# Kernel optimization log

Hardware: AMD Instinct MI355X
Metric: run time of the kernel (lower is better)

The kernel has to match this reference:

```python
import jax, jax.numpy as jnp
import numpy as np

B, D_IN, D_H, D_OUT = 1024, 1024, 4096, 1024
SPARSITY = 0.5  # fraction of weights KEPT (top-k)


def setup_inputs() -> dict:
    key = jax.random.key(0)
    ks = jax.random.split(key, 13)
    def kaiming(k, shape):
        fan_in = shape[-1] if len(shape) > 1 else shape[0]
        bound = 1.0 / np.sqrt(fan_in)
        return jax.random.uniform(k, shape, jnp.float32, -bound, bound)
    inp = {
        "x":   jax.random.normal(ks[0], (B, D_IN), jnp.float32),
        "W1":  kaiming(ks[1], (D_H, D_IN)),
        "b1":  kaiming(ks[2], (D_H,)),
        "W2":  kaiming(ks[3], (D_H, D_H)),
        "b2":  kaiming(ks[4], (D_H,)),
        "W3":  kaiming(ks[5], (D_OUT, D_H)),
        "b3":  kaiming(ks[6], (D_OUT,)),
        # scores: kaiming-uniform for weights, N(0, 0.01) for biases (as in Mask.__init__)
        "sW1": kaiming(ks[7], (D_H, D_IN)),
        "sb1": 0.01 * jax.random.normal(ks[8], (D_H,), jnp.float32),
        "sW2": kaiming(ks[9], (D_H, D_H)),
        "sb2": 0.01 * jax.random.normal(ks[10], (D_H,), jnp.float32),
        "sW3": kaiming(ks[11], (D_OUT, D_H)),
        "sb3": 0.01 * jax.random.normal(ks[12], (D_OUT,), jnp.float32),
    }
    return inp


def _global_masks(scores):
    """Single fused global top-k threshold mask (replaces O(P) redundant sorts).
    Bottom (1-SPARSITY) fraction (by value rank) -> 0, top SPARSITY fraction -> 1."""
    flat = jnp.concatenate([s.ravel() for s in scores])
    n = flat.shape[0]
    j = int((1.0 - SPARSITY) * n)  # number of zeroed entries
    idx = jnp.argsort(flat)
    bin_mask = jnp.zeros((n,), flat.dtype).at[idx[j:]].set(1.0)
    # straight-through: d(mask)/d(score) = 1 (GetSubnet_global.backward returns g)
    st_mask = bin_mask + flat - jax.lax.stop_gradient(flat)
    sizes = [int(np.prod(s.shape)) for s in scores]
    offs = np.concatenate([[0], np.cumsum(sizes)])
    return [st_mask[offs[i]:offs[i + 1]].reshape(scores[i].shape)
            for i in range(len(scores))]


def reference(x, W1, b1, W2, b2, W3, b3, sW1, sb1, sW2, sb2, sW3, sb3):
    masks = _global_masks([sW1, sb1, sW2, sb2, sW3, sb3])
    mW1, mb1, mW2, mb2, mW3, mb3 = masks
    # masked params, then MLP forward (torch Linear: y = x @ W.T + b)
    h = jax.nn.relu(x @ (W1 * mW1).T + b1 * mb1)
    h = jax.nn.relu(h @ (W2 * mW2).T + b2 * mb2)
    return h @ (W3 * mW3).T + b3 * mb3
```

## Files before the change

kernel.cpp:

```cpp
#include <hip/hip_runtime.h>
#include <hip/hip_bf16.h>
#include <stdint.h>


typedef __bf16 bf16_t;
typedef __bf16 bf16x4 __attribute__((ext_vector_type(4)));
typedef __bf16 bf16x8 __attribute__((ext_vector_type(8)));
typedef float  f32x4  __attribute__((ext_vector_type(4)));

using gvoid = const __attribute__((address_space(1))) void;
using svoid = __attribute__((address_space(3))) void;

#define O1 4194304L
#define O2 4198400L
#define O3 20975616L
#define O4 20979712L
#define O5 25174016L
#define N_TOT 25175040L
#define J_RANK 12587520u
#define CAND_CAP 4096

#define WS_HIST 0u
#define WS_RES  32768u
#define WS_CNT  32784u
#define WS_CAND 32800u
#define WS_W1B  131072u
#define WS_B1F  8519680u
#define WS_W2B  8536064u
#define WS_B2F  42090496u
#define WS_W3B  42106880u
#define WS_B3F  50495488u
#define WS_H1F  50511872u
#define WS_H2F  58900480u
#define WS_FAST_END 67289088ull
#define WS_H1   131072u
#define WS_H2   8519680u

#define SWZ(row, chunk) ((((chunk) + ((row) >> 1)) & 3))

__device__ __forceinline__ unsigned int mono32(float f) {
    unsigned int u = __float_as_uint(f);
    return (u & 0x80000000u) ? ~u : (u | 0x80000000u);
}

__global__ __launch_bounds__(256) void zero_kernel(unsigned int* p, int n) {
    int i = blockIdx.x * 256 + threadIdx.x;
    if (i < n) p[i] = 0u;
}

__device__ __forceinline__ void seg_lookup(long e,
    const float* s0, const float* s1, const float* s2,
    const float* s3, const float* s4, const float* s5,
    const float** sp, long* off) {
    if (e < O1)      { *sp = s0; *off = e; }
    else if (e < O2) { *sp = s1; *off = e - O1; }
    else if (e < O3) { *sp = s2; *off = e - O2; }
    else if (e < O4) { *sp = s3; *off = e - O3; }
    else if (e < O5) { *sp = s4; *off = e - O4; }
    else             { *sp = s5; *off = e - O5; }
}

__global__ __launch_bounds__(256) void hist_kernel(
    const float* s0, const float* s1, const float* s2,
    const float* s3, const float* s4, const float* s5,
    unsigned int* hist) {
    __shared__ unsigned int lh[8192];
    for (int i = threadIdx.x; i < 8192; i += 256) lh[i] = 0u;
    __syncthreads();
    const long ng = N_TOT / 4;
    for (long g = (long)blockIdx.x * 256 + threadIdx.x; g < ng;
         g += (long)gridDim.x * 256) {
        long e = g * 4;
        const float* sp; long o;
        seg_lookup(e, s0, s1, s2, s3, s4, s5, &sp, &o);
        float4 v = *(const float4*)(sp + o);
        atomicAdd(&lh[mono32(v.x) >> 19], 1u);
        atomicAdd(&lh[mono32(v.y) >> 19], 1u);
        atomicAdd(&lh[mono32(v.z) >> 19], 1u);
        atomicAdd(&lh[mono32(v.w) >> 19], 1u);
    }
    __syncthreads();
    for (int i = threadIdx.x; i < 8192; i += 256) {
        unsigned int c = lh[i];
        if (c) atomicAdd(&hist[i], c);
    }
}

__global__ __launch_bounds__(256) void select_kernel(const unsigned int* hist,
                                                     unsigned int* res) {
    __shared__ unsigned int part[256];
    int tid = threadIdx.x;
    unsigned int s = 0;
    for (int b = tid * 32; b < tid * 32 + 32; ++b) s += hist[b];
    part[tid] = s;
    __syncthreads();
    if (tid == 0) {
        unsigned int acc = 0;
        for (int i = 0; i < 256; ++i) { unsigned int v = part[i]; part[i] = acc; acc += v; }
    }
    __syncthreads();
    unsigned int acc = part[tid];
    for (int b = tid * 32; b < tid * 32 + 32; ++b) {
        unsigned int h = hist[b];
        if (acc <= J_RANK && J_RANK < acc + h) {
            res[0] = (unsigned int)b;
            res[1] = acc;
            res[2] = J_RANK - acc;
        }
        acc += h;
    }
}

__global__ __launch_bounds__(256) void mask_apply_fast(
    const float* s0, const float* s1, const float* s2,
    const float* s3, const float* s4, const float* s5,
    const float* w0, const float* w1, const float* w2,
    const float* w3, const float* w4, const float* w5,
    bf16_t* W1b, float* b1f, bf16_t* W2b, float* b2f, bf16_t* W3b, float* b3f,
    const unsigned int* res, unsigned int* cand_cnt, unsigned long long* cand) {
    const unsigned int C = res[0];
    const long ng = N_TOT / 4;
    for (long g = (long)blockIdx.x * 256 + threadIdx.x; g < ng;
         g += (long)gridDim.x * 256) {
        long e = g * 4;
        const float* sp; long o;
        seg_lookup(e, s0, s1, s2, s3, s4, s5, &sp, &o);
        const float* wp;
        if (e < O1)      wp = w0;
        else if (e < O2) wp = w1;
        else if (e < O3) wp = w2;
        else if (e < O4) wp = w3;
        else if (e < O5) wp = w4;
        else             wp = w5;
        float4 sv = *(const float4*)(sp + o);
        float4 wv = *(const float4*)(wp + o);
#define PROC(comp, ci)                                                         \
        { unsigned int key = mono32(sv.comp); unsigned int kb = key >> 19;     \
          if (kb < C) wv.comp = 0.f;                                           \
          else if (kb == C) {                                                  \
              unsigned int slot = atomicAdd(cand_cnt, 1u);                     \
              if (slot < CAND_CAP)                                             \
                  cand[slot] = (((unsigned long long)key) << 32) |             \
                               (unsigned long long)(unsigned int)(e + ci);     \
          } }
        PROC(x, 0) PROC(y, 1) PROC(z, 2) PROC(w, 3)
#undef PROC
        if (e < O1) {
            bf16x4 b; b[0]=(__bf16)wv.x; b[1]=(__bf16)wv.y; b[2]=(__bf16)wv.z; b[3]=(__bf16)wv.w;
            *(bf16x4*)(W1b + o) = b;
        } else if (e < O2) {
            *(float4*)(b1f + o) = wv;
        } else if (e < O3) {
            bf16x4 b; b[0]=(__bf16)wv.x; b[1]=(__bf16)wv.y; b[2]=(__bf16)wv.z; b[3]=(__bf16)wv.w;
            *(bf16x4*)(W2b + o) = b;
        } else if (e < O4) {
            *(float4*)(b2f + o) = wv;
        } else if (e < O5) {
            bf16x4 b; b[0]=(__bf16)wv.x; b[1]=(__bf16)wv.y; b[2]=(__bf16)wv.z; b[3]=(__bf16)wv.w;
            *(bf16x4*)(W3b + o) = b;
        } else {
            *(float4*)(b3f + o) = wv;
        }
    }
}

__global__ __launch_bounds__(256) void finalize_fast(
    const unsigned int* res, const unsigned int* cand_cnt,
    const unsigned long long* cand,
    bf16_t* W1b, float* b1f, bf16_t* W2b, float* b2f, bf16_t* W3b, float* b3f) {
    __shared__ unsigned long long buf[CAND_CAP];
    int tid = threadIdx.x;
    unsigned int cnt = *cand_cnt; if (cnt > CAND_CAP) cnt = CAND_CAP;
    unsigned int need = res[2];   if (need > cnt) need = cnt;
    for (int i = tid; i < (int)cnt; i += 256) buf[i] = cand[i];
    __syncthreads();
    for (int i = tid; i < (int)cnt; i += 256) {
        unsigned long long me = buf[i];
        unsigned int rank = 0;
        for (unsigned int j = 0; j < cnt; ++j) rank += (buf[j] < me);
        if (rank < need) {
            long idx = (long)(unsigned int)(me & 0xFFFFFFFFu);
            if (idx < O1)      W1b[idx] = (__bf16)0.f;
            else if (idx < O2) b1f[idx - O1] = 0.f;
            else if (idx < O3) W2b[idx - O2] = (__bf16)0.f;
            else if (idx < O4) b2f[idx - O3] = 0.f;
            else if (idx < O5) W3b[idx - O4] = (__bf16)0.f;
            else               b3f[idx - O5] = 0.f;
        }
    }
}

__global__ __launch_bounds__(256) void mask_apply_kernel(
    const float* s0, const float* s1, const float* s2,
    const float* s3, const float* s4, const float* s5,
    float* w0, float* w1, float* w2, float* w3, float* w4, float* w5,
    const unsigned int* res, unsigned int* cand_cnt, unsigned long long* cand) {
    const unsigned int C = res[0];
    const long ng = N_TOT / 4;
    for (long g = (long)blockIdx.x * 256 + threadIdx.x; g < ng;
         g += (long)gridDim.x * 256) {
        long e = g * 4;
        const float* sp; long o;
        seg_lookup(e, s0, s1, s2, s3, s4, s5, &sp, &o);
        float* wp;
        if (e < O1)      wp = w0;
        else if (e < O2) wp = w1;
        else if (e < O3) wp = w2;
        else if (e < O4) wp = w3;
        else if (e < O5) wp = w4;
        else             wp = w5;
        float4 sv = *(const float4*)(sp + o);
        float4 wv = *(float4*)(wp + o);
#define PROC(comp, ci)                                                         \
        { unsigned int key = mono32(sv.comp); unsigned int kb = key >> 19;     \
          if (kb < C) wv.comp = 0.f;                                           \
          else if (kb == C) {                                                  \
              unsigned int slot = atomicAdd(cand_cnt, 1u);                     \
              if (slot < CAND_CAP)                                             \
                  cand[slot] = (((unsigned long long)key) << 32) |             \
                               (unsigned long long)(unsigned int)(e + ci);     \
          } }
        PROC(x, 0) PROC(y, 1) PROC(z, 2) PROC(w, 3)
#undef PROC
        *(float4*)(wp + o) = wv;
    }
}

__global__ __launch_bounds__(256) void finalize_kernel(
    const unsigned int* res, const unsigned int* cand_cnt,
    const unsigned long long* cand,
    float* w0, float* w1, float* w2, float* w3, float* w4, float* w5) {
    __shared__ unsigned long long buf[CAND_CAP];
    int tid = threadIdx.x;
    unsigned int cnt = *cand_cnt; if (cnt > CAND_CAP) cnt = CAND_CAP;
    unsigned int need = res[2];   if (need > cnt) need = cnt;
    for (int i = tid; i < (int)cnt; i += 256) buf[i] = cand[i];
    __syncthreads();
    for (int i = tid; i < (int)cnt; i += 256) {
        unsigned long long me = buf[i];
        unsigned int rank = 0;
        for (unsigned int j = 0; j < cnt; ++j) rank += (buf[j] < me);
        if (rank < need) {
            long idx = (long)(unsigned int)(me & 0xFFFFFFFFu);
            if (idx < O1)      w0[idx] = 0.f;
            else if (idx < O2) w1[idx - O1] = 0.f;
            else if (idx < O3) w2[idx - O2] = 0.f;
            else if (idx < O4) w3[idx - O3] = 0.f;
            else if (idx < O5) w4[idx - O4] = 0.f;
            else               w5[idx - O5] = 0.f;
        }
    }
}

__device__ __forceinline__ bf16x8 load8(const float* p) {
    float4 a = *(const float4*)p;
    float4 b = *(const float4*)(p + 4);
    bf16x8 r;
    r[0] = (__bf16)a.x; r[1] = (__bf16)a.y; r[2] = (__bf16)a.z; r[3] = (__bf16)a.w;
    r[4] = (__bf16)b.x; r[5] = (__bf16)b.y; r[6] = (__bf16)b.z; r[7] = (__bf16)b.w;
    return r;
}
__device__ __forceinline__ bf16x8 load8(const bf16_t* p) {
    return *(const bf16x8*)p;
}

template <int BM, int BN, bool RELU, typename TA, typename TB, typename TC>
__global__ __launch_bounds__(256) void gemm_bt(
    const TA* __restrict__ A, const TB* __restrict__ B,
    const float* __restrict__ bias, TC* __restrict__ C,
    int M, int N, int K) {
    constexpr int BK = 32;
    constexpr int WM = BM / 2, WN = BN / 2;
    constexpr int TM = WM / 16, TN = WN / 16;
    constexpr int CA = (BM * BK) / 8;
    constexpr int CB = (BN * BK) / 8;
    __shared__ __align__(16) bf16_t As[BM * BK];
    __shared__ __align__(16) bf16_t Bs[BN * BK];

    const int tid = threadIdx.x;
    const int w = tid >> 6, lane = tid & 63;
    const int quad = lane >> 4, l16 = lane & 15;
    const int wm = (w >> 1) * WM, wn = (w & 1) * WN;
    const int rowBase = blockIdx.y * BM;
    const int colBase = blockIdx.x * BN;

    f32x4 acc[TM][TN] = {};

    const TA* Ab = A + (size_t)rowBase * K;
    const TB* Bb = B + (size_t)colBase * K;

    for (int k0 = 0; k0 < K; k0 += BK) {
        __syncthreads();
#pragma unroll
        for (int c0 = 0; c0 < CA; c0 += 256) {
            int c = c0 + tid;
            int row = c >> 2, kc = c & 3;
            *(bf16x8*)&As[row * BK + SWZ(row, kc) * 8] =
                load8(Ab + (size_t)row * K + k0 + kc * 8);
        }
#pragma unroll
        for (int c0 = 0; c0 < CB; c0 += 256) {
            int c = c0 + tid;
            int row = c >> 2, kc = c & 3;
            *(bf16x8*)&Bs[row * BK + SWZ(row, kc) * 8] =
                load8(Bb + (size_t)row * K + k0 + kc * 8);
        }
        __syncthreads();
        bf16x8 af[TM], bfr[TN];
#pragma unroll
        for (int i = 0; i < TM; ++i) {
            int r = wm + i * 16 + l16;
            af[i] = *(const bf16x8*)&As[r * BK + SWZ(r, quad) * 8];
        }
#pragma unroll
        for (int j = 0; j < TN; ++j) {
            int r = wn + j * 16 + l16;
            bfr[j] = *(const bf16x8*)&Bs[r * BK + SWZ(r, quad) * 8];
        }
#pragma unroll
        for (int i = 0; i < TM; ++i)
#pragma unroll
            for (int j = 0; j < TN; ++j)
                acc[i][j] = __builtin_amdgcn_mfma_f32_16x16x32_bf16(
                    af[i], bfr[j], acc[i][j], 0, 0, 0);
    }

#pragma unroll
    for (int i = 0; i < TM; ++i) {
#pragma unroll
        for (int j = 0; j < TN; ++j) {
            int col = colBase + wn + j * 16 + l16;
            float bv = bias[col];
#pragma unroll
            for (int r = 0; r < 4; ++r) {
                int rowg = rowBase + wm + i * 16 + quad * 4 + r;
                float v = acc[i][j][r] + bv;
                if (RELU) v = v > 0.f ? v : 0.f;
                if constexpr (sizeof(TC) == 4)
                    C[(size_t)rowg * N + col] = v;
                else
                    C[(size_t)rowg * N + col] = (bf16_t)v;
            }
        }
    }
}

template <int BM, int BN, bool RELU, int SPLITK, typename TA, typename TC>
__global__ __launch_bounds__(256) void gemm_fast(
    const TA* __restrict__ A, const bf16_t* __restrict__ B,
    const float* __restrict__ bias, TC* __restrict__ C,
    int M, int N, int K) {
    constexpr int BK = 32;
    constexpr int WM = BM / 2, WN = BN / 2;
    constexpr int TM = WM / 16, TN = WN / 16;
    constexpr int CA = (BM * BK) / 8;
    constexpr int CB = (BN * BK) / 8;
    __shared__ __align__(16) bf16_t As[BM * BK];
    __shared__ __align__(16) bf16_t Bs[BN * BK];

    const int tid = threadIdx.x;
    const int w = tid >> 6, lane = tid & 63;
    const int quad = lane >> 4, l16 = lane & 15;
    const int wm = (w >> 1) * WM, wn = (w & 1) * WN;
    const int rowBase = blockIdx.y * BM;
    const int colBase = blockIdx.x * BN;

    f32x4 acc[TM][TN] = {};

    const TA* Ab = A + (size_t)rowBase * K;
    const bf16_t* Bb = B + (size_t)colBase * K;

    const int kPart = K / SPLITK;
    const int kBeg = (SPLITK > 1) ? (int)blockIdx.z * kPart : 0;

    for (int k0 = kBeg; k0 < kBeg + kPart; k0 += BK) {
        if constexpr (sizeof(TA) == 2) {
#pragma unroll
            for (int c0 = 0; c0 < CA; c0 += 256) {
                int c = c0 + tid;
                int row = c >> 2, phys = c & 3;
                int lc = (phys - (row >> 1)) & 3;
                __builtin_amdgcn_global_load_lds(
                    (gvoid*)(Ab + (size_t)row * K + k0 + lc * 8),
                    (svoid*)(As + c * 8), 16, 0, 0);
            }
        } else {
#pragma unroll
            for (int c0 = 0; c0 < CA; c0 += 256) {
                int c = c0 + tid;
                int row = c >> 2, kc = c & 3;
                *(bf16x8*)&As[row * BK + SWZ(row, kc) * 8] =
                    load8(Ab + (size_t)row * K + k0 + kc * 8);
            }
        }
#pragma unroll
        for (int c0 = 0; c0 < CB; c0 += 256) {
            int c = c0 + tid;
            int row = c >> 2, phys = c & 3;
            int lc = (phys - (row >> 1)) & 3;
            __builtin_amdgcn_global_load_lds(
                (gvoid*)(Bb + (size_t)row * K + k0 + lc * 8),
                (svoid*)(Bs + c * 8), 16, 0, 0);
        }
        __syncthreads();

        bf16x8 af[TM], bfr[TN];
#pragma unroll
        for (int i = 0; i < TM; ++i) {
            int r = wm + i * 16 + l16;
            af[i] = *(const bf16x8*)&As[r * BK + SWZ(r, quad) * 8];
        }
#pragma unroll
        for (int j = 0; j < TN; ++j) {
            int r = wn + j * 16 + l16;
            bfr[j] = *(const bf16x8*)&Bs[r * BK + SWZ(r, quad) * 8];
        }
#pragma unroll
        for (int i = 0; i < TM; ++i)
#pragma unroll
            for (int j = 0; j < TN; ++j)
                acc[i][j] = __builtin_amdgcn_mfma_f32_16x16x32_bf16(
                    af[i], bfr[j], acc[i][j], 0, 0, 0);
        __syncthreads();
    }

#pragma unroll
    for (int i = 0; i < TM; ++i) {
#pragma unroll
        for (int j = 0; j < TN; ++j) {
            int col = colBase + wn + j * 16 + l16;
            float bv = (SPLITK == 1 || blockIdx.z == 0) ? bias[col] : 0.f;
#pragma unroll
            for (int r = 0; r < 4; ++r) {
                int rowg = rowBase + wm + i * 16 + quad * 4 + r;
                float v = acc[i][j][r] + bv;
                if constexpr (SPLITK == 1) {
                    if (RELU) v = v > 0.f ? v : 0.f;
                    if constexpr (sizeof(TC) == 4)
                        C[(size_t)rowg * N + col] = v;
                    else
                        C[(size_t)rowg * N + col] = (bf16_t)v;
                } else {
                    atomicAdd((float*)&C[(size_t)rowg * N + col], v);
                }
            }
        }
    }
}

extern "C" void kernel_launch(void* const* d_in, const int* in_sizes, int n_in,
                              void* d_out, int out_size, void* d_ws, size_t ws_size,
                              hipStream_t stream) {
    const float* x  = (const float*)d_in[0];
    float* W1 = (float*)d_in[1];
    float* b1 = (float*)d_in[2];
    float* W2 = (float*)d_in[3];
    float* b2 = (float*)d_in[4];
    float* W3 = (float*)d_in[5];
    float* b3 = (float*)d_in[6];
    const float* s0 = (const float*)d_in[7];
    const float* s1 = (const float*)d_in[8];
    const float* s2 = (const float*)d_in[9];
    const float* s3 = (const float*)d_in[10];
    const float* s4 = (const float*)d_in[11];
    const float* s5 = (const float*)d_in[12];

    uint8_t* ws = (uint8_t*)d_ws;
    unsigned int* hist = (unsigned int*)(ws + WS_HIST);
    unsigned int* res  = (unsigned int*)(ws + WS_RES);
    unsigned int* cnt  = (unsigned int*)(ws + WS_CNT);
    unsigned long long* cand = (unsigned long long*)(ws + WS_CAND);
    float* OUT = (float*)d_out;

    zero_kernel<<<33, 256, 0, stream>>>((unsigned int*)ws, 8200);
    hist_kernel<<<1024, 256, 0, stream>>>(s0, s1, s2, s3, s4, s5, hist);
    select_kernel<<<1, 256, 0, stream>>>(hist, res);

    if (ws_size >= WS_FAST_END) {
        bf16_t* W1b = (bf16_t*)(ws + WS_W1B);
        float*  b1f = (float*)(ws + WS_B1F);
        bf16_t* W2b = (bf16_t*)(ws + WS_W2B);
        float*  b2f = (float*)(ws + WS_B2F);
        bf16_t* W3b = (bf16_t*)(ws + WS_W3B);
        float*  b3f = (float*)(ws + WS_B3F);
        bf16_t* H1  = (bf16_t*)(ws + WS_H1F);
        bf16_t* H2  = (bf16_t*)(ws + WS_H2F);
        zero_kernel<<<4096, 256, 0, stream>>>((unsigned int*)OUT, 1048576);
        mask_apply_fast<<<2048, 256, 0, stream>>>(
            s0, s1, s2, s3, s4, s5, W1, b1, W2, b2, W3, b3,
            W1b, b1f, W2b, b2f, W3b, b3f, res, cnt, cand);
        finalize_fast<<<1, 256, 0, stream>>>(res, cnt, cand,
                                             W1b, b1f, W2b, b2f, W3b, b3f);
        gemm_fast<64, 128, true, 1, float, bf16_t>
            <<<dim3(32, 16), 256, 0, stream>>>(x, W1b, b1f, H1, 1024, 4096, 1024);
        gemm_fast<64, 128, true, 1, bf16_t, bf16_t>
            <<<dim3(32, 16), 256, 0, stream>>>(H1, W2b, b2f, H2, 1024, 4096, 4096);
        gemm_fast<64, 128, false, 4, bf16_t, float>
            <<<dim3(8, 16, 4), 256, 0, stream>>>(H2, W3b, b3f, OUT, 1024, 1024, 4096);
    } else {
        bf16_t* H1 = (bf16_t*)(ws + WS_H1);
        bf16_t* H2 = (bf16_t*)(ws + WS_H2);
        mask_apply_kernel<<<2048, 256, 0, stream>>>(s0, s1, s2, s3, s4, s5,
                                                    W1, b1, W2, b2, W3, b3,
                                                    res, cnt, cand);
        finalize_kernel<<<1, 256, 0, stream>>>(res, cnt, cand,
                                               W1, b1, W2, b2, W3, b3);
        gemm_bt<64, 128, true, float, float, bf16_t>
            <<<dim3(32, 16), 256, 0, stream>>>(x, W1, b1, H1, 1024, 4096, 1024);
        gemm_bt<64, 128, true, bf16_t, float, bf16_t>
            <<<dim3(32, 16), 256, 0, stream>>>(H1, W2, b2, H2, 1024, 4096, 4096);
        gemm_bt<64, 64, false, bf16_t, float, float>
            <<<dim3(16, 16), 256, 0, stream>>>(H2, W3, b3, OUT, 1024, 1024, 4096);
    }
}
```

Measured before the change: 410.7 us.

## Triple-buffer GEMM LDS tiles with async global-to-LDS prefetch and pre-convert x to bf16

Replaces the single-buffered GEMM main loop with a three-stage LDS ring. Global-to-LDS loads for tile t+2 are issued before computing tile t, and explicit vmcnt waits plus one barrier per step replace the two __syncthreads. This is meant to hide global memory latency behind MFMA work. A separate kernel converts x to bf16 first so the first GEMM can also use async LDS loads; it reuses the H2 buffer as scratch, which is safe only because H2 is written after the first GEMM runs. The change adds a launch, triples LDS use, and hardcodes vmcnt immediates that assume exactly three loads per thread per step.

```diff
diff --git a/kernel.cpp b/kernel.cpp
--- a/kernel.cpp
+++ b/kernel.cpp
@@ -46,6 +46,19 @@
 __global__ __launch_bounds__(256) void zero_kernel(unsigned int* p, int n) {
     int i = blockIdx.x * 256 + threadIdx.x;
     if (i < n) p[i] = 0u;
+}
+
+__global__ __launch_bounds__(256) void cvt_x_kernel(const float* __restrict__ x,
+                                                    bf16_t* __restrict__ xb, int n8) {
+    int i = blockIdx.x * 256 + threadIdx.x;
+    if (i < n8) {
+        const float4 a = *(const float4*)(x + (size_t)i * 8);
+        const float4 b = *(const float4*)(x + (size_t)i * 8 + 4);
+        bf16x8 r;
+        r[0] = (__bf16)a.x; r[1] = (__bf16)a.y; r[2] = (__bf16)a.z; r[3] = (__bf16)a.w;
+        r[4] = (__bf16)b.x; r[5] = (__bf16)b.y; r[6] = (__bf16)b.z; r[7] = (__bf16)b.w;
+        *(bf16x8*)(xb + (size_t)i * 8) = r;
+    }
 }
 
 __device__ __forceinline__ void seg_lookup(long e,
@@ -345,9 +358,9 @@
     }
 }
 
-template <int BM, int BN, bool RELU, int SPLITK, typename TA, typename TC>
-__global__ __launch_bounds__(256) void gemm_fast(
-    const TA* __restrict__ A, const bf16_t* __restrict__ B,
+template <int BM, int BN, bool RELU, int SPLITK, typename TC>
+__global__ __launch_bounds__(256) void gemm_pipe(
+    const bf16_t* __restrict__ A, const bf16_t* __restrict__ B,
     const float* __restrict__ bias, TC* __restrict__ C,
     int M, int N, int K) {
     constexpr int BK = 32;
@@ -355,8 +368,9 @@
     constexpr int TM = WM / 16, TN = WN / 16;
     constexpr int CA = (BM * BK) / 8;
     constexpr int CB = (BN * BK) / 8;
-    __shared__ __align__(16) bf16_t As[BM * BK];
-    __shared__ __align__(16) bf16_t Bs[BN * BK];
+    static_assert(CA == 256 && CB == 512, "vmcnt immediates assume 3 loads/thread/step");
+    __shared__ __align__(16) bf16_t As[3][BM * BK];
+    __shared__ __align__(16) bf16_t Bs[3][BN * BK];
 
     const int tid = threadIdx.x;
     const int w = tid >> 6, lane = tid & 63;
@@ -367,53 +381,43 @@
 
     f32x4 acc[TM][TN] = {};
 
-    const TA* Ab = A + (size_t)rowBase * K;
+    const bf16_t* Ab = A + (size_t)rowBase * K;
     const bf16_t* Bb = B + (size_t)colBase * K;
 
     const int kPart = K / SPLITK;
     const int kBeg = (SPLITK > 1) ? (int)blockIdx.z * kPart : 0;
-
-    for (int k0 = kBeg; k0 < kBeg + kPart; k0 += BK) {
-        if constexpr (sizeof(TA) == 2) {
-#pragma unroll
-            for (int c0 = 0; c0 < CA; c0 += 256) {
-                int c = c0 + tid;
-                int row = c >> 2, phys = c & 3;
-                int lc = (phys - (row >> 1)) & 3;
-                __builtin_amdgcn_global_load_lds(
-                    (gvoid*)(Ab + (size_t)row * K + k0 + lc * 8),
-                    (svoid*)(As + c * 8), 16, 0, 0);
-            }
-        } else {
-#pragma unroll
-            for (int c0 = 0; c0 < CA; c0 += 256) {
-                int c = c0 + tid;
-                int row = c >> 2, kc = c & 3;
-                *(bf16x8*)&As[row * BK + SWZ(row, kc) * 8] =
-                    load8(Ab + (size_t)row * K + k0 + kc * 8);
-            }
-        }
-#pragma unroll
-        for (int c0 = 0; c0 < CB; c0 += 256) {
-            int c = c0 + tid;
-            int row = c >> 2, phys = c & 3;
-            int lc = (phys - (row >> 1)) & 3;
-            __builtin_amdgcn_global_load_lds(
-                (gvoid*)(Bb + (size_t)row * K + k0 + lc * 8),
-                (svoid*)(Bs + c * 8), 16, 0, 0);
-        }
-        __syncthreads();
-
+    const int nt = kPart / BK;
+
+    const int rowA = tid >> 2;
+    const int lcA  = ((tid & 3) - (rowA >> 1)) & 3;
+    const bf16_t* aSrc = Ab + (size_t)rowA * K + lcA * 8;
+    const int rowB0 = tid >> 2;
+    const int lcB0  = ((tid & 3) - (rowB0 >> 1)) & 3;
+    const int cB1   = tid + 256;
+    const int rowB1 = cB1 >> 2;
+    const int lcB1  = ((cB1 & 3) - (rowB1 >> 1)) & 3;
+    const bf16_t* bSrc0 = Bb + (size_t)rowB0 * K + lcB0 * 8;
+    const bf16_t* bSrc1 = Bb + (size_t)rowB1 * K + lcB1 * 8;
+
+    auto stage = [&](int buf, int k0) {
+        __builtin_amdgcn_global_load_lds((gvoid*)(aSrc + k0),
+            (svoid*)(As[buf] + tid * 8), 16, 0, 0);
+        __builtin_amdgcn_global_load_lds((gvoid*)(bSrc0 + k0),
+            (svoid*)(Bs[buf] + tid * 8), 16, 0, 0);
+        __builtin_amdgcn_global_load_lds((gvoid*)(bSrc1 + k0),
+            (svoid*)(Bs[buf] + (size_t)cB1 * 8), 16, 0, 0);
+    };
+    auto compute = [&](int buf) {
         bf16x8 af[TM], bfr[TN];
 #pragma unroll
         for (int i = 0; i < TM; ++i) {
             int r = wm + i * 16 + l16;
-            af[i] = *(const bf16x8*)&As[r * BK + SWZ(r, quad) * 8];
+            af[i] = *(const bf16x8*)&As[buf][r * BK + SWZ(r, quad) * 8];
         }
 #pragma unroll
         for (int j = 0; j < TN; ++j) {
             int r = wn + j * 16 + l16;
-            bfr[j] = *(const bf16x8*)&Bs[r * BK + SWZ(r, quad) * 8];
+            bfr[j] = *(const bf16x8*)&Bs[buf][r * BK + SWZ(r, quad) * 8];
         }
 #pragma unroll
         for (int i = 0; i < TM; ++i)
@@ -421,8 +425,27 @@
             for (int j = 0; j < TN; ++j)
                 acc[i][j] = __builtin_amdgcn_mfma_f32_16x16x32_bf16(
                     af[i], bfr[j], acc[i][j], 0, 0, 0);
-        __syncthreads();
-    }
+    };
+
+    stage(0, kBeg);
+    stage(1, kBeg + BK);
+    asm volatile("s_waitcnt vmcnt(3)" ::: "memory");
+    __builtin_amdgcn_s_barrier();
+    __builtin_amdgcn_sched_barrier(0);
+
+    int k0 = kBeg;
+    for (int t = 0; t < nt - 2; ++t, k0 += BK) {
+        stage((t + 2) % 3, k0 + 2 * BK);
+        compute(t % 3);
+        asm volatile("s_waitcnt vmcnt(3)" ::: "memory");
+        __builtin_amdgcn_s_barrier();
+        __builtin_amdgcn_sched_barrier(0);
+    }
+    compute((nt - 2) % 3);
+    asm volatile("s_waitcnt vmcnt(0)" ::: "memory");
+    __builtin_amdgcn_s_barrier();
+    __builtin_amdgcn_sched_barrier(0);
+    compute((nt - 1) % 3);
 
 #pragma unroll
     for (int i = 0; i < TM; ++i) {
@@ -485,17 +508,19 @@
         float*  b3f = (float*)(ws + WS_B3F);
         bf16_t* H1  = (bf16_t*)(ws + WS_H1F);
         bf16_t* H2  = (bf16_t*)(ws + WS_H2F);
+        bf16_t* xb  = (bf16_t*)(ws + WS_H2F);
         zero_kernel<<<4096, 256, 0, stream>>>((unsigned int*)OUT, 1048576);
+        cvt_x_kernel<<<512, 256, 0, stream>>>(x, xb, 131072);
         mask_apply_fast<<<2048, 256, 0, stream>>>(
             s0, s1, s2, s3, s4, s5, W1, b1, W2, b2, W3, b3,
             W1b, b1f, W2b, b2f, W3b, b3f, res, cnt, cand);
         finalize_fast<<<1, 256, 0, stream>>>(res, cnt, cand,
                                              W1b, b1f, W2b, b2f, W3b, b3f);
-        gemm_fast<64, 128, true, 1, float, bf16_t>
-            <<<dim3(32, 16), 256, 0, stream>>>(x, W1b, b1f, H1, 1024, 4096, 1024);
-        gemm_fast<64, 128, true, 1, bf16_t, bf16_t>
+        gemm_pipe<64, 128, true, 1, bf16_t>
+            <<<dim3(32, 16), 256, 0, stream>>>(xb, W1b, b1f, H1, 1024, 4096, 1024);
+        gemm_pipe<64, 128, true, 1, bf16_t>
             <<<dim3(32, 16), 256, 0, stream>>>(H1, W2b, b2f, H2, 1024, 4096, 4096);
-        gemm_fast<64, 128, false, 4, bf16_t, float>
+        gemm_pipe<64, 128, false, 4, float>
             <<<dim3(8, 16, 4), 256, 0, stream>>>(H2, W3b, b3f, OUT, 1024, 1024, 4096);
     } else {
         bf16_t* H1 = (bf16_t*)(ws + WS_H1);
```

After: 389.8 us. -5.1%, faster.
